# Kernel optimization log

Hardware: AMD Instinct MI355X
Metric: run time of the kernel (lower is better)

## Reference

```python
import jax, jax.numpy as jnp
import numpy as np

B, N, D, H = 2, 160, 4096, 4
DH = D // H            # dim_head = 1024
SCALE = DH ** -0.5     # applied twice, as in the torch module


def setup_inputs() -> dict:
    key = jax.random.key(0)
    k1, k2, k3, k4 = jax.random.split(key, 4)
    w_std = 0.02
    return {
        "x": jax.random.normal(k1, (B, N, D), jnp.float32),
        "y": jax.random.normal(k2, (B, N, D), jnp.float32),
        "Wq": jax.random.normal(k3, (D, D), jnp.float32) * w_std,  # to_Q weight (out,in)
        "Wk": jax.random.normal(k4, (D, D), jnp.float32) * w_std,  # to_K weight (out,in)
    }


def reference(x, y, Wq, Wk):
    # q = to_Q(y): (B, N, D); torch Linear computes y @ W^T
    q = y @ Wq.T
    # k = to_K(x) split into heads: (B, H, N, DH)
    k = (x @ Wk.T).reshape(B, N, H, DH).transpose(0, 2, 1, 3)
    # kkt[b,h,i,j] = sum_d k[b,h,i,d] * k[b,h,j,d], scaled -> (B, H, N, N)
    kkt = jnp.einsum('bhid,bhjd->bhij', k, k) * SCALE
    # q is replicated across heads in the original (repeat), so contract
    # directly with the head-free q: dots[b,h,i,j] = sum_m q[b,m,i] * kkt[b,h,j,m]
    # -> (B, H, D, N), scaled again
    dots = jnp.einsum('bmi,bhjm->bhij', q, kkt) * SCALE
    attn = jax.nn.softplus(dots)
    # flatten(1) then reshape(40, 32, D): row-major, so a single reshape
    return attn.reshape(40, 32, D)
```

## Files before the change

kernel.cpp:

```cpp
#include <hip/hip_runtime.h>
#include <hip/hip_bf16.h>


typedef __attribute__((ext_vector_type(4))) float  f32x4;
typedef __attribute__((ext_vector_type(8))) __bf16 bf16x8;

#define SCALE 0.03125f

static __device__ __forceinline__ f32x4 mfma16(bf16x8 a, bf16x8 b, f32x4 c) {
    return __builtin_amdgcn_mfma_f32_16x16x32_bf16(a, b, c, 0, 0, 0);
}

static __device__ __forceinline__ bf16x8 pack8(f32x4 a, f32x4 b) {
    bf16x8 r;
    #pragma unroll
    for (int i = 0; i < 4; ++i) { r[i] = (__bf16)a[i]; r[4 + i] = (__bf16)b[i]; }
    return r;
}

static __device__ __forceinline__ bf16x8 pack8f(const float* v) {
    bf16x8 r;
    #pragma unroll
    for (int i = 0; i < 8; ++i) r[i] = (__bf16)v[i];
    return r;
}

static __device__ __forceinline__ float softplus(float x) {
    return fmaxf(x, 0.0f) + log1pf(expf(-fabsf(x)));
}

__global__ __launch_bounds__(256)
void cvt_kernel(const float* __restrict__ x, const float* __restrict__ y,
                __bf16* __restrict__ xb, __bf16* __restrict__ yb)
{
    const float* src = blockIdx.y ? y : x;
    __bf16* dst = blockIdx.y ? yb : xb;
    size_t i = ((size_t)blockIdx.x * 256 + threadIdx.x) * 8;
    f32x4 a = __builtin_nontemporal_load((const f32x4*)(src + i));
    f32x4 b = __builtin_nontemporal_load((const f32x4*)(src + i + 4));
    *(bf16x8*)(dst + i) = pack8(a, b);
}

__global__ __launch_bounds__(256, 2)
void qk_gemm(const __bf16* __restrict__ yb, const __bf16* __restrict__ xb,
             const float* __restrict__ Wq, const float* __restrict__ Wk,
             __bf16* __restrict__ P)
{
    const int key = blockIdx.x & 7;
    const int z   = key >> 2;
    const int ks  = key & 3;
    const int np  = blockIdx.x >> 3;
    const int bn  = np * 64;
    const int kc  = ks * 1024;

    __shared__ __bf16 lA[320 * 64];
    __shared__ __bf16 lW[64 * 64];

    const int tid  = threadIdx.x;
    const int lane = tid & 63;
    const int wid  = tid >> 6;
    const int li   = lane & 15;
    const int lk   = lane >> 4;

    const __bf16* __restrict__ Ab = z ? xb : yb;
    const float*  __restrict__ Wm = z ? Wk : Wq;

    const int arow  = tid >> 3;
    const int aslot = tid & 7;
    const int aswz  = (aslot ^ (arow & 7)) * 8;
    const __bf16* ag = Ab + (size_t)arow * 4096 + kc + aslot * 8;

    const int wrow = tid >> 2;
    const float* wg = Wm + (size_t)(bn + wrow) * 4096 + kc + (tid & 3) * 16;
    const int wsl0 = ((((tid & 3) << 1))     ^ (wrow & 7)) * 8;
    const int wsl1 = ((((tid & 3) << 1) | 1) ^ (wrow & 7)) * 8;

    f32x4 acc[5][4] = {};
    bf16x8 areg[10];
    f32x4  wreg[4];

    #pragma unroll
    for (int p = 0; p < 10; ++p)
        areg[p] = *(const bf16x8*)(ag + (size_t)p * 32 * 4096);
    #pragma unroll
    for (int i = 0; i < 4; ++i)
        wreg[i] = __builtin_nontemporal_load((const f32x4*)(wg + i * 4));

    for (int s = 0; s < 16; ++s) {
        __syncthreads();
        #pragma unroll
        for (int p = 0; p < 10; ++p)
            *(bf16x8*)&lA[(p * 32 + arow) * 64 + aswz] = areg[p];
        *(bf16x8*)&lW[wrow * 64 + wsl0] = pack8(wreg[0], wreg[1]);
        *(bf16x8*)&lW[wrow * 64 + wsl1] = pack8(wreg[2], wreg[3]);
        __syncthreads();

        if (s < 15) {
            #pragma unroll
            for (int p = 0; p < 10; ++p)
                areg[p] = *(const bf16x8*)(ag + (size_t)p * 32 * 4096 + (s + 1) * 64);
            #pragma unroll
            for (int i = 0; i < 4; ++i)
                wreg[i] = __builtin_nontemporal_load((const f32x4*)(wg + (s + 1) * 64 + i * 4));
        }

        #pragma unroll
        for (int kk = 0; kk < 2; ++kk) {
            const int slot = kk * 4 + lk;
            bf16x8 wf[4], af[5];
            #pragma unroll
            for (int jn = 0; jn < 4; ++jn) {
                const int j = jn * 16 + li;
                wf[jn] = *(const bf16x8*)&lW[j * 64 + ((slot ^ (j & 7)) << 3)];
            }
            #pragma unroll
            for (int m = 0; m < 5; ++m) {
                const int rr = wid * 80 + m * 16 + li;
                af[m] = *(const bf16x8*)&lA[rr * 64 + ((slot ^ (rr & 7)) << 3)];
            }
            __builtin_amdgcn_s_setprio(1);
            #pragma unroll
            for (int m = 0; m < 5; ++m)
                #pragma unroll
                for (int jn = 0; jn < 4; ++jn)
                    acc[m][jn] = mfma16(af[m], wf[jn], acc[m][jn]);
            __builtin_amdgcn_s_setprio(0);
        }
    }

    __bf16* Pz = P + (size_t)key * 320 * 4096;
    #pragma unroll
    for (int m = 0; m < 5; ++m) {
        const int row0 = wid * 80 + m * 16 + lk * 4;
        #pragma unroll
        for (int jn = 0; jn < 4; ++jn) {
            const int col = bn + jn * 16 + li;
            #pragma unroll
            for (int r = 0; r < 4; ++r)
                __builtin_nontemporal_store((__bf16)acc[m][jn][r],
                                            &Pz[(size_t)(row0 + r) * 4096 + col]);
        }
    }
}

__global__ __launch_bounds__(256)
void reduce_kernel(const __bf16* __restrict__ P,
                   __bf16* __restrict__ qT, __bf16* __restrict__ kout)
{
    const int z    = blockIdx.z;
    const int col0 = blockIdx.x * 64;
    const int row0 = blockIdx.y * 64;
    const __bf16* P0 = P + ((size_t)z * 4 + 0) * 320 * 4096;
    const __bf16* P1 = P + ((size_t)z * 4 + 1) * 320 * 4096;
    const __bf16* P2 = P + ((size_t)z * 4 + 2) * 320 * 4096;
    const __bf16* P3 = P + ((size_t)z * 4 + 3) * 320 * 4096;

    const int t  = threadIdx.x;
    const int r  = t >> 2;
    const int cc = (t & 3) * 16;

    float v[16];
    {
        size_t base = (size_t)(row0 + r) * 4096 + col0 + cc;
        #pragma unroll
        for (int i = 0; i < 2; ++i) {
            bf16x8 a = *(const bf16x8*)(P0 + base + i * 8);
            bf16x8 b = *(const bf16x8*)(P1 + base + i * 8);
            bf16x8 c = *(const bf16x8*)(P2 + base + i * 8);
            bf16x8 d = *(const bf16x8*)(P3 + base + i * 8);
            #pragma unroll
            for (int j = 0; j < 8; ++j)
                v[i * 8 + j] = (float)a[j] + (float)b[j] + (float)c[j] + (float)d[j];
        }
    }

    if (z == 1) {
        __bf16* dst = kout + (size_t)(row0 + r) * 4096 + col0 + cc;
        *(bf16x8*)dst       = pack8f(v);
        *(bf16x8*)(dst + 8) = pack8f(v + 8);
        return;
    }

    __shared__ float lt[64][65];
    #pragma unroll
    for (int i = 0; i < 16; ++i) lt[r][cc + i] = v[i];
    __syncthreads();

    const int col = t & 63;
    const int rr0 = (t >> 6) * 16;
    float w[16];
    #pragma unroll
    for (int i = 0; i < 16; ++i) w[i] = lt[rr0 + i][col];

    const int gr = row0 + rr0;
    const int b  = gr >= 160;
    const int ri = gr - b * 160;
    __bf16* dst = qT + (size_t)b * 4096 * 160 + (size_t)(col0 + col) * 160 + ri;
    *(bf16x8*)dst       = pack8f(w);
    *(bf16x8*)(dst + 8) = pack8f(w + 8);
}

__global__ __launch_bounds__(64)
void kkt_kernel(const __bf16* __restrict__ kmat, __bf16* __restrict__ kkt)
{
    const int bh = blockIdx.x;
    const int b  = bh >> 2, h = bh & 3;
    const int i0 = blockIdx.y * 16;
    const int j0 = blockIdx.z * 16;
    const int lane = threadIdx.x;

    const __bf16* base = kmat + (size_t)b * 160 * 4096 + h * 1024;
    const int ko = (lane >> 4) << 3;
    const __bf16* pa = base + (size_t)(i0 + (lane & 15)) * 4096 + ko;
    const __bf16* pb = base + (size_t)(j0 + (lane & 15)) * 4096 + ko;

    f32x4 acc = {};
    #pragma unroll 4
    for (int kk = 0; kk < 1024; kk += 32) {
        bf16x8 a  = *(const bf16x8*)(pa + kk);
        bf16x8 bb = *(const bf16x8*)(pb + kk);
        acc = mfma16(a, bb, acc);
    }

    #pragma unroll
    for (int r = 0; r < 4; ++r) {
        int i = i0 + ((lane >> 4) << 2) + r;
        int j = j0 + (lane & 15);
        kkt[((size_t)bh * 160 + i) * 160 + j] = (__bf16)(acc[r] * SCALE);
    }
}

__global__ __launch_bounds__(256)
void dots_kernel(const __bf16* __restrict__ qT, const __bf16* __restrict__ kkt,
                 float* __restrict__ out)
{
    const int bh   = blockIdx.z;
    const int b    = bh >> 2;
    const int lane = threadIdx.x & 63;
    const int wid  = threadIdx.x >> 6;
    const int i0   = blockIdx.x * 64 + wid * 16;
    const int j0   = blockIdx.y * 32;

    const __bf16* Ab = qT + (size_t)b * 4096 * 160;
    const __bf16* Bb = kkt + (size_t)bh * 160 * 160;
    const int ko = (lane >> 4) << 3;
    const __bf16* pa  = Ab + (size_t)(i0 + (lane & 15)) * 160 + ko;
    const __bf16* pb0 = Bb + (size_t)(j0 + (lane & 15)) * 160 + ko;
    const __bf16* pb1 = pb0 + 16 * 160;

    f32x4 acc0 = {}, acc1 = {};
    #pragma unroll
    for (int m0 = 0; m0 < 160; m0 += 32) {
        bf16x8 a  = *(const bf16x8*)(pa + m0);
        bf16x8 b0 = *(const bf16x8*)(pb0 + m0);
        bf16x8 b1 = *(const bf16x8*)(pb1 + m0);
        acc0 = mfma16(a, b0, acc0);
        acc1 = mfma16(a, b1, acc1);
    }

    #pragma unroll
    for (int r = 0; r < 4; ++r) {
        int i = i0 + ((lane >> 4) << 2) + r;
        int j = j0 + (lane & 15);
        size_t o = ((size_t)bh * 4096 + i) * 160 + j;
        __builtin_nontemporal_store(softplus(acc0[r] * SCALE), &out[o]);
        __builtin_nontemporal_store(softplus(acc1[r] * SCALE), &out[o + 16]);
    }
}

extern "C" void kernel_launch(void* const* d_in, const int* in_sizes, int n_in,
                              void* d_out, int out_size, void* d_ws, size_t ws_size,
                              hipStream_t stream)
{
    const float* x  = (const float*)d_in[0];
    const float* y  = (const float*)d_in[1];
    const float* Wq = (const float*)d_in[2];
    const float* Wk = (const float*)d_in[3];
    float* out = (float*)d_out;

    __bf16* qT  = (__bf16*)d_ws;
    __bf16* kbf = qT  + (size_t)2 * 4096 * 160;
    __bf16* kkt = kbf + (size_t)320 * 4096;
    __bf16* xb  = kkt + (size_t)8 * 160 * 160;
    __bf16* yb  = xb  + (size_t)320 * 4096;
    __bf16* P   = yb  + (size_t)320 * 4096;

    cvt_kernel   <<<dim3(640, 2),    256, 0, stream>>>(x, y, xb, yb);
    qk_gemm      <<<dim3(512),       256, 0, stream>>>(yb, xb, Wq, Wk, P);
    reduce_kernel<<<dim3(64, 5, 2),  256, 0, stream>>>(P, qT, kbf);
    kkt_kernel   <<<dim3(8, 10, 10),  64, 0, stream>>>(kbf, kkt);
    dots_kernel  <<<dim3(64, 5, 8),  256, 0, stream>>>(qT, kkt, out);
}
```

Baseline: 112.5 us.

## Restructure qk_gemm: narrower N tiles, direct global A fragments, double-buffered W LDS

```diff
diff --git a/kernel.cpp b/kernel.cpp
--- a/kernel.cpp
+++ b/kernel.cpp
@@ -4,6 +4,7 @@
 
 typedef __attribute__((ext_vector_type(4))) float  f32x4;
 typedef __attribute__((ext_vector_type(8))) __bf16 bf16x8;
+typedef __attribute__((ext_vector_type(4))) __bf16 bf16x4;
 
 #define SCALE 0.03125f
 
@@ -36,12 +37,12 @@
     const float* src = blockIdx.y ? y : x;
     __bf16* dst = blockIdx.y ? yb : xb;
     size_t i = ((size_t)blockIdx.x * 256 + threadIdx.x) * 8;
-    f32x4 a = __builtin_nontemporal_load((const f32x4*)(src + i));
-    f32x4 b = __builtin_nontemporal_load((const f32x4*)(src + i + 4));
+    f32x4 a = *(const f32x4*)(src + i);
+    f32x4 b = *(const f32x4*)(src + i + 4);
     *(bf16x8*)(dst + i) = pack8(a, b);
 }
 
-__global__ __launch_bounds__(256, 2)
+__global__ __launch_bounds__(256, 4)
 void qk_gemm(const __bf16* __restrict__ yb, const __bf16* __restrict__ xb,
              const float* __restrict__ Wq, const float* __restrict__ Wk,
              __bf16* __restrict__ P)
@@ -50,11 +51,10 @@
     const int z   = key >> 2;
     const int ks  = key & 3;
     const int np  = blockIdx.x >> 3;
-    const int bn  = np * 64;
+    const int bn  = np * 32;
     const int kc  = ks * 1024;
 
-    __shared__ __bf16 lA[320 * 64];
-    __shared__ __bf16 lW[64 * 64];
+    __shared__ __bf16 lW[2][32 * 256];
 
     const int tid  = threadIdx.x;
     const int lane = tid & 63;
@@ -65,66 +65,77 @@
     const __bf16* __restrict__ Ab = z ? xb : yb;
     const float*  __restrict__ Wm = z ? Wk : Wq;
 
-    const int arow  = tid >> 3;
-    const int aslot = tid & 7;
-    const int aswz  = (aslot ^ (arow & 7)) * 8;
-    const __bf16* ag = Ab + (size_t)arow * 4096 + kc + aslot * 8;
-
-    const int wrow = tid >> 2;
-    const float* wg = Wm + (size_t)(bn + wrow) * 4096 + kc + (tid & 3) * 16;
-    const int wsl0 = ((((tid & 3) << 1))     ^ (wrow & 7)) * 8;
-    const int wsl1 = ((((tid & 3) << 1) | 1) ^ (wrow & 7)) * 8;
-
-    f32x4 acc[5][4] = {};
-    bf16x8 areg[10];
-    f32x4  wreg[4];
-
-    #pragma unroll
-    for (int p = 0; p < 10; ++p)
-        areg[p] = *(const bf16x8*)(ag + (size_t)p * 32 * 4096);
-    #pragma unroll
-    for (int i = 0; i < 4; ++i)
-        wreg[i] = __builtin_nontemporal_load((const f32x4*)(wg + i * 4));
-
-    for (int s = 0; s < 16; ++s) {
+    const float* wbase = Wm + (size_t)(bn + wid * 8) * 4096 + kc + lane * 4;
+
+    const __bf16* ap[5];
+    #pragma unroll
+    for (int m = 0; m < 5; ++m)
+        ap[m] = Ab + (size_t)(wid * 80 + m * 16 + li) * 4096 + kc + lk * 8;
+
+    f32x4  wfetch[8];
+    f32x4  acc[5][2] = {};
+
+    #pragma unroll
+    for (int rr = 0; rr < 8; ++rr)
+        wfetch[rr] = __builtin_nontemporal_load((const f32x4*)(wbase + (size_t)rr * 4096));
+    #pragma unroll
+    for (int rr = 0; rr < 8; ++rr) {
+        const int r = wid * 8 + rr;
+        bf16x4 v; v[0] = (__bf16)wfetch[rr][0]; v[1] = (__bf16)wfetch[rr][1];
+                  v[2] = (__bf16)wfetch[rr][2]; v[3] = (__bf16)wfetch[rr][3];
+        char* d = (char*)&lW[0][0] + r * 512 + (((lane >> 1) ^ (r & 7)) << 4)
+                + (lane & 1) * 8;
+        *(bf16x4*)d = v;
+    }
+    __syncthreads();
+
+    for (int c = 0; c < 4; ++c) {
+        if (c < 3) {
+            #pragma unroll
+            for (int rr = 0; rr < 8; ++rr)
+                wfetch[rr] = __builtin_nontemporal_load(
+                    (const f32x4*)(wbase + (size_t)rr * 4096 + (c + 1) * 256));
+        }
+
+        const char* lwb = (const char*)&lW[c & 1][0];
+        #pragma unroll
+        for (int s = 0; s < 4; ++s) {
+            #pragma unroll
+            for (int kk = 0; kk < 2; ++kk) {
+                const int kg = c * 256 + s * 64 + kk * 32;
+                bf16x8 af[5];
+                #pragma unroll
+                for (int m = 0; m < 5; ++m)
+                    af[m] = *(const bf16x8*)(ap[m] + kg);
+                const int slot = s * 8 + kk * 4 + lk;
+                bf16x8 wf[2];
+                #pragma unroll
+                for (int jn = 0; jn < 2; ++jn) {
+                    const int j = jn * 16 + li;
+                    wf[jn] = *(const bf16x8*)(lwb + j * 512 + ((slot ^ (j & 7)) << 4));
+                }
+                __builtin_amdgcn_s_setprio(1);
+                #pragma unroll
+                for (int m = 0; m < 5; ++m) {
+                    acc[m][0] = mfma16(af[m], wf[0], acc[m][0]);
+                    acc[m][1] = mfma16(af[m], wf[1], acc[m][1]);
+                }
+                __builtin_amdgcn_s_setprio(0);
+            }
+        }
+
         __syncthreads();
-        #pragma unroll
-        for (int p = 0; p < 10; ++p)
-            *(bf16x8*)&lA[(p * 32 + arow) * 64 + aswz] = areg[p];
-        *(bf16x8*)&lW[wrow * 64 + wsl0] = pack8(wreg[0], wreg[1]);
-        *(bf16x8*)&lW[wrow * 64 + wsl1] = pack8(wreg[2], wreg[3]);
-        __syncthreads();
-
-        if (s < 15) {
-            #pragma unroll
-            for (int p = 0; p < 10; ++p)
-                areg[p] = *(const bf16x8*)(ag + (size_t)p * 32 * 4096 + (s + 1) * 64);
-            #pragma unroll
-            for (int i = 0; i < 4; ++i)
-                wreg[i] = __builtin_nontemporal_load((const f32x4*)(wg + (s + 1) * 64 + i * 4));
-        }
-
-        #pragma unroll
-        for (int kk = 0; kk < 2; ++kk) {
-            const int slot = kk * 4 + lk;
-            bf16x8 wf[4], af[5];
-            #pragma unroll
-            for (int jn = 0; jn < 4; ++jn) {
-                const int j = jn * 16 + li;
-                wf[jn] = *(const bf16x8*)&lW[j * 64 + ((slot ^ (j & 7)) << 3)];
+        if (c < 3) {
+            #pragma unroll
+            for (int rr = 0; rr < 8; ++rr) {
+                const int r = wid * 8 + rr;
+                bf16x4 v; v[0] = (__bf16)wfetch[rr][0]; v[1] = (__bf16)wfetch[rr][1];
+                          v[2] = (__bf16)wfetch[rr][2]; v[3] = (__bf16)wfetch[rr][3];
+                char* d = (char*)&lW[(c + 1) & 1][0] + r * 512
+                        + (((lane >> 1) ^ (r & 7)) << 4) + (lane & 1) * 8;
+                *(bf16x4*)d = v;
             }
-            #pragma unroll
-            for (int m = 0; m < 5; ++m) {
-                const int rr = wid * 80 + m * 16 + li;
-                af[m] = *(const bf16x8*)&lA[rr * 64 + ((slot ^ (rr & 7)) << 3)];
-            }
-            __builtin_amdgcn_s_setprio(1);
-            #pragma unroll
-            for (int m = 0; m < 5; ++m)
-                #pragma unroll
-                for (int jn = 0; jn < 4; ++jn)
-                    acc[m][jn] = mfma16(af[m], wf[jn], acc[m][jn]);
-            __builtin_amdgcn_s_setprio(0);
+            __syncthreads();
         }
     }
 
@@ -133,12 +144,11 @@
     for (int m = 0; m < 5; ++m) {
         const int row0 = wid * 80 + m * 16 + lk * 4;
         #pragma unroll
-        for (int jn = 0; jn < 4; ++jn) {
+        for (int jn = 0; jn < 2; ++jn) {
             const int col = bn + jn * 16 + li;
             #pragma unroll
             for (int r = 0; r < 4; ++r)
-                __builtin_nontemporal_store((__bf16)acc[m][jn][r],
-                                            &Pz[(size_t)(row0 + r) * 4096 + col]);
+                Pz[(size_t)(row0 + r) * 4096 + col] = (__bf16)acc[m][jn][r];
         }
     }
 }
@@ -263,8 +273,8 @@
         int i = i0 + ((lane >> 4) << 2) + r;
         int j = j0 + (lane & 15);
         size_t o = ((size_t)bh * 4096 + i) * 160 + j;
-        __builtin_nontemporal_store(softplus(acc0[r] * SCALE), &out[o]);
-        __builtin_nontemporal_store(softplus(acc1[r] * SCALE), &out[o + 16]);
+        out[o]      = softplus(acc0[r] * SCALE);
+        out[o + 16] = softplus(acc1[r] * SCALE);
     }
 }
 
@@ -286,7 +296,7 @@
     __bf16* P   = yb  + (size_t)320 * 4096;
 
     cvt_kernel   <<<dim3(640, 2),    256, 0, stream>>>(x, y, xb, yb);
-    qk_gemm      <<<dim3(512),       256, 0, stream>>>(yb, xb, Wq, Wk, P);
+    qk_gemm      <<<dim3(1024),      256, 0, stream>>>(yb, xb, Wq, Wk, P);
     reduce_kernel<<<dim3(64, 5, 2),  256, 0, stream>>>(P, qT, kbf);
     kkt_kernel   <<<dim3(8, 10, 10),  64, 0, stream>>>(kbf, kkt);
     dots_kernel  <<<dim3(64, 5, 8),  256, 0, stream>>>(qT, kkt, out);
```

After: 152.8 us (median of 2 runs). 1.36x slower.
